# Performance work log

Hardware: AMD Instinct MI355X
Metric: run time of the kernel (lower is better)

The kernel has to match this reference:

```python
import jax, jax.numpy as jnp
import numpy as np

B, N, D_MODEL = 16, 65536, 512
NBUCKETS = 11
BN_EPS = 1e-5
LN_EPS = 1e-5


def setup_inputs() -> dict:
    key = jax.random.key(0)
    ks = jax.random.split(key, 12)
    def w(k, shape, fan_in):
        return jax.random.normal(k, shape, jnp.float32) * (1.0 / np.sqrt(fan_in))
    return {
        "x": jax.random.normal(ks[0], (B, N, 3), jnp.float32),
        "w1": w(ks[1], (3, 64), 3),   "b1": jnp.zeros((64,), jnp.float32),
        "g1": jnp.ones((64,), jnp.float32),  "be1": jnp.zeros((64,), jnp.float32),
        "w2": w(ks[2], (64, 128), 64), "b2": jnp.zeros((128,), jnp.float32),
        "g2": jnp.ones((128,), jnp.float32), "be2": jnp.zeros((128,), jnp.float32),
        "w3": w(ks[3], (128, 256), 128), "b3": jnp.zeros((256,), jnp.float32),
        "g3": jnp.ones((256,), jnp.float32), "be3": jnp.zeros((256,), jnp.float32),
        "wp": w(ks[4], (518, D_MODEL), 518), "bp": jnp.zeros((D_MODEL,), jnp.float32),
        "g_ln": jnp.ones((D_MODEL,), jnp.float32), "b_ln": jnp.zeros((D_MODEL,), jnp.float32),
    }


def _bn(h, g, b):
    # BatchNorm1d in training mode: biased variance over the flattened batch axis
    m = jnp.mean(h, axis=0)
    v = jnp.mean((h - m) ** 2, axis=0)
    return (h - m) * jax.lax.rsqrt(v + BN_EPS) * g + b


def reference(x, w1, b1, g1, be1, w2, b2, g2, be2, w3, b3, g3, be3, wp, bp, g_ln, b_ln):
    Bb, Nn, _ = x.shape
    x_flat = x.reshape(Bb * Nn, 3)
    h = jax.nn.relu(_bn(x_flat @ w1 + b1, g1, be1))
    h = jax.nn.relu(_bn(h @ w2 + b2, g2, be2))
    h = jax.nn.relu(_bn(h @ w3 + b3, g3, be3))
    feat = h.reshape(Bb, Nn, 256)

    # y-bucket histogram means of (x, z) coordinates, vectorized via segment_sum
    y = x[:, :, 1]
    y_min = jnp.min(y, axis=1, keepdims=True)
    y_max = jnp.max(y, axis=1, keepdims=True)
    y_norm = (y - y_min) / (y_max - y_min + 1e-6)
    buckets = jnp.clip((y_norm * 10).astype(jnp.int32), 0, NBUCKETS - 1)  # (B,N) in [0,10]
    seg = (jnp.arange(Bb, dtype=jnp.int32)[:, None] * NBUCKETS + buckets).reshape(-1)
    nseg = Bb * NBUCKETS
    sx = jax.ops.segment_sum(x[:, :, 0].reshape(-1), seg, num_segments=nseg)
    sz = jax.ops.segment_sum(x[:, :, 2].reshape(-1), seg, num_segments=nseg)
    cnt = jax.ops.segment_sum(jnp.ones((Bb * Nn,), jnp.float32), seg, num_segments=nseg)
    denom = jnp.maximum(cnt, 1.0)
    cx = (sx / denom).reshape(Bb, NBUCKETS)
    cz = (sz / denom).reshape(Bb, NBUCKETS)
    x_centers = jnp.take_along_axis(cx, buckets, axis=1)  # (B,N)
    z_centers = jnp.take_along_axis(cz, buckets, axis=1)

    dx = x[:, :, 0] - x_centers
    dz = x[:, :, 2] - z_centers
    theta = jnp.arctan2(dz, dx)
    r = jnp.sqrt(dx ** 2 + dz ** 2)
    spatial = jnp.stack([jnp.sin(theta), jnp.cos(theta), r], axis=-1)  # (B,N,3)

    feat = jnp.concatenate([feat, spatial], axis=-1)  # (B,N,259)
    feat_max = jnp.max(feat, axis=1)
    feat_avg = jnp.mean(feat, axis=1)
    feat_cat = jnp.concatenate([feat_max, feat_avg], axis=1)  # (B,518)

    out = feat_cat @ wp + bp
    mu = jnp.mean(out, axis=-1, keepdims=True)
    var = jnp.mean((out - mu) ** 2, axis=-1, keepdims=True)
    return (out - mu) * jax.lax.rsqrt(var + LN_EPS) * g_ln + b_ln
```

## Files before the change

kernel.cpp:

```cpp
#include <hip/hip_runtime.h>
#include <stdint.h>

#define B_    16
#define N_    65536
#define NPTS  (B_*N_)
#define NBK   11
#define NFEAT 259
#define NF    ((float)NPTS)

typedef float f32x4 __attribute__((ext_vector_type(4)));
typedef short s16x8 __attribute__((ext_vector_type(8)));
union frag_u { s16x8 v; unsigned u[4]; };
union x24_u  { float4 v4[6]; float f[24]; };

enum {
  OFF_YMINF = 16,
  OFF_YMAXF = 32,
  OFF_A1    = 64,
  OFF_C1    = 128,
  OFF_A2    = 192,
  OFF_C2    = 320,
  OFF_CX    = 448,
  OFF_CZ    = 624,
  OFF_A3    = 800,
  OFF_C3    = 1056,
  OFF_GC    = 2048,
  OFF_G1S   = 6144,
  OFF_H3C   = 6400,
  OFF_PSTR  = 16384,
  OFF_PBKT  = 24576,
  OFF_PSPA  = 43008,
  OFF_PG    = 49152,
  OFF_PGS   = 2146304,
  OFF_PH3   = 2179072,
  OFF_PPOOL = 3227648
};

__device__ __forceinline__ float wave_sum(float v){
  #pragma unroll
  for (int m=32;m>=1;m>>=1) v += __shfl_xor(v,m,64);
  return v;
}
__device__ __forceinline__ float wave_max(float v){
  #pragma unroll
  for (int m=32;m>=1;m>>=1) v = fmaxf(v,__shfl_xor(v,m,64));
  return v;
}
__device__ __forceinline__ float wave_min(float v){
  #pragma unroll
  for (int m=32;m>=1;m>>=1) v = fminf(v,__shfl_xor(v,m,64));
  return v;
}
__device__ __forceinline__ unsigned short bf16_bits(float f){
  unsigned u=__float_as_uint(f);
  u += 0x7FFFu + ((u>>16)&1u);
  return (unsigned short)(u>>16);
}
__device__ __forceinline__ unsigned cvt_pk_bf16(float lo, float hi){
  unsigned r;
  asm("v_cvt_pk_bf16_f32 %0, %1, %2" : "=v"(r) : "v"(lo), "v"(hi));
  return r;
}

__global__ __launch_bounds__(256) void k_stream0(const float* __restrict__ x,
                                                 float* __restrict__ ws){
  __shared__ float red[4][12];
  const int t=threadIdx.x, l=t&63, w=t>>6;
  const int bid=blockIdx.x;
  const float4* xv=(const float4*)(x + (size_t)bid*2048*3);
  float s0=0,s1=0,s2=0,q00=0,q01=0,q02=0,q11=0,q12=0,q22=0;
  float ymn=3.4e38f, ymx=-3.4e38f;
  #pragma unroll
  for (int i=0;i<2;i++){
    const int vi=(i*256+t)*3;
    const float4 a=xv[vi], b4=xv[vi+1], c=xv[vi+2];
    float X[4]={a.x,a.w,b4.z,c.y};
    float Y[4]={a.y,b4.x,b4.w,c.z};
    float Z[4]={a.z,b4.y,c.x,c.w};
    #pragma unroll
    for (int p=0;p<4;p++){
      s0+=X[p]; s1+=Y[p]; s2+=Z[p];
      q00=fmaf(X[p],X[p],q00); q01=fmaf(X[p],Y[p],q01); q02=fmaf(X[p],Z[p],q02);
      q11=fmaf(Y[p],Y[p],q11); q12=fmaf(Y[p],Z[p],q12); q22=fmaf(Z[p],Z[p],q22);
      ymn=fminf(ymn,Y[p]); ymx=fmaxf(ymx,Y[p]);
    }
  }
  s0=wave_sum(s0); s1=wave_sum(s1); s2=wave_sum(s2);
  q00=wave_sum(q00); q01=wave_sum(q01); q02=wave_sum(q02);
  q11=wave_sum(q11); q12=wave_sum(q12); q22=wave_sum(q22);
  ymn=wave_min(ymn); ymx=wave_max(ymx);
  if (l==0){
    red[w][0]=s0; red[w][1]=s1; red[w][2]=s2;
    red[w][3]=q00; red[w][4]=q01; red[w][5]=q02;
    red[w][6]=q11; red[w][7]=q12; red[w][8]=q22;
    red[w][9]=ymn; red[w][10]=ymx;
  }
  __syncthreads();
  if (t<11){
    const float v0=red[0][t],v1=red[1][t],v2=red[2][t],v3=red[3][t];
    float r;
    if (t==9)       r=fminf(fminf(v0,v1),fminf(v2,v3));
    else if (t==10) r=fmaxf(fmaxf(v0,v1),fmaxf(v2,v3));
    else            r=v0+v1+v2+v3;
    ws[OFF_PSTR+bid*16+t]=r;
  }
}

__global__ void k_finA(const float* __restrict__ w1, const float* __restrict__ b1,
                       const float* __restrict__ gm, const float* __restrict__ bt,
                       float* __restrict__ ws){
  __shared__ float sums[9];
  const int t=threadIdx.x;
  if (t<9){
    float s=0.f;
    #pragma unroll 8
    for (int blk=0;blk<512;blk++) s+=ws[OFF_PSTR+blk*16+t];
    sums[t]=s;
  }
  if (t>=32&&t<48){
    const int b=t-32; float m=3.4e38f;
    #pragma unroll 8
    for (int blk=0;blk<32;blk++) m=fminf(m,ws[OFF_PSTR+(b*32+blk)*16+9]);
    ws[OFF_YMINF+b]=m;
  }
  if (t>=48&&t<64){
    const int b=t-48; float m=-3.4e38f;
    #pragma unroll 8
    for (int blk=0;blk<32;blk++) m=fmaxf(m,ws[OFF_PSTR+(b*32+blk)*16+10]);
    ws[OFF_YMAXF+b]=m;
  }
  __syncthreads();
  if (t<64){
    const float i_n=1.f/NF;
    const float w0=w1[t], wa=w1[64+t], wb=w1[128+t];
    const float ms=(w0*sums[0]+wa*sums[1]+wb*sums[2])*i_n;
    const float es=(w0*w0*sums[3]+wa*wa*sums[6]+wb*wb*sums[8]
                   +2.f*(w0*wa*sums[4]+w0*wb*sums[5]+wa*wb*sums[7]))*i_n;
    const float var=es-ms*ms;
    const float a=gm[t]/sqrtf(var+1e-5f);
    ws[OFF_A1+t]=a; ws[OFF_C1+t]=bt[t]-(ms+b1[t])*a;
  }
}

__global__ __launch_bounds__(256) void k_bucket(const float* __restrict__ x,
                                                float* __restrict__ ws){
  __shared__ float red[4][12];
  const int t=threadIdx.x, l=t&63, w=t>>6;
  const int bid=blockIdx.x, b=bid>>5;
  const float ymn=ws[OFF_YMINF+b], ymx=ws[OFF_YMAXF+b];
  const float4* xv=(const float4*)(x + (size_t)bid*2048*3);
  float sxl[NBK], szl[NBK], cntl[NBK];
  #pragma unroll
  for (int k=0;k<NBK;k++){ sxl[k]=0.f; szl[k]=0.f; cntl[k]=0.f; }
  #pragma unroll
  for (int i=0;i<2;i++){
    const int vi=(i*256+t)*3;
    const float4 a=xv[vi], b4=xv[vi+1], c=xv[vi+2];
    float X[4]={a.x,a.w,b4.z,c.y};
    float Y[4]={a.y,b4.x,b4.w,c.z};
    float Z[4]={a.z,b4.y,c.x,c.w};
    #pragma unroll
    for (int p=0;p<4;p++){
      const float yn=(Y[p]-ymn)/(ymx-ymn+1e-6f);
      int bk=(int)(yn*10.f); bk = bk<0?0:(bk>10?10:bk);
      #pragma unroll
      for (int k=0;k<NBK;k++){
        const bool m=(bk==k);
        sxl[k]+= m?X[p]:0.f; szl[k]+= m?Z[p]:0.f; cntl[k]+= m?1.f:0.f;
      }
    }
  }
  #pragma unroll
  for (int k=0;k<NBK;k++){
    const float s=wave_sum(sxl[k]);
    if (l==0) red[w][k]=s;
  }
  __syncthreads();
  if (t<NBK) ws[OFF_PBKT+bid*36+t]=red[0][t]+red[1][t]+red[2][t]+red[3][t];
  __syncthreads();
  #pragma unroll
  for (int k=0;k<NBK;k++){
    const float z=wave_sum(szl[k]);
    if (l==0) red[w][k]=z;
  }
  __syncthreads();
  if (t<NBK) ws[OFF_PBKT+bid*36+11+t]=red[0][t]+red[1][t]+red[2][t]+red[3][t];
  __syncthreads();
  #pragma unroll
  for (int k=0;k<NBK;k++){
    const float c=wave_sum(cntl[k]);
    if (l==0) red[w][k]=c;
  }
  __syncthreads();
  if (t<NBK) ws[OFF_PBKT+bid*36+22+t]=red[0][t]+red[1][t]+red[2][t]+red[3][t];
}

__global__ __launch_bounds__(256) void k_spatial(const float* __restrict__ x,
                                                 float* __restrict__ ws){
  __shared__ float red[4][8];
  const int t=threadIdx.x, l=t&63, w=t>>6;
  const int bid=blockIdx.x, b=bid>>5;
  const float ymn=ws[OFF_YMINF+b], ymx=ws[OFF_YMAXF+b];
  const float4* xv=(const float4*)(x + (size_t)bid*2048*3);
  float mx[3]={-3.4e38f,-3.4e38f,-3.4e38f}, sm[3]={0.f,0.f,0.f};
  #pragma unroll
  for (int i=0;i<2;i++){
    const int vi=(i*256+t)*3;
    const float4 a=xv[vi], b4=xv[vi+1], c=xv[vi+2];
    float X[4]={a.x,a.w,b4.z,c.y};
    float Y[4]={a.y,b4.x,b4.w,c.z};
    float Z[4]={a.z,b4.y,c.x,c.w};
    #pragma unroll
    for (int p=0;p<4;p++){
      const float yn=(Y[p]-ymn)/(ymx-ymn+1e-6f);
      int bk=(int)(yn*10.f); bk = bk<0?0:(bk>10?10:bk);
      const float dx=X[p]-ws[OFF_CX+b*NBK+bk];
      const float dz=Z[p]-ws[OFF_CZ+b*NBK+bk];
      const float r=sqrtf(fmaf(dx,dx,dz*dz));
      const float sn=(r>0.f)?(dz/r):0.f;
      const float cs=(r>0.f)?(dx/r):1.f;
      mx[0]=fmaxf(mx[0],sn); sm[0]+=sn;
      mx[1]=fmaxf(mx[1],cs); sm[1]+=cs;
      mx[2]=fmaxf(mx[2],r);  sm[2]+=r;
// ... 60 lines not shown
    if (!(w&1)){
      #pragma unroll
      for (int j=0;j<8;j++) s1+=gA[j];
    }
  }
  #pragma unroll
  for (int q=0;q<4;q++){
    ws[OFF_PG + (size_t)((16*ti+4*lg+q)*64 + 16*tj0+lr)*512 + bid]=acc0[q];
    ws[OFF_PG + (size_t)((16*ti+4*lg+q)*64 + 16*tj1+lr)*512 + bid]=acc1[q];
  }
  if (!(w&1)){
    s1+=__shfl_xor(s1,16); s1+=__shfl_xor(s1,32);
    if (l<16) ws[OFF_PGS + (16*ti+lr)*512 + bid]=s1;
  }
}

__global__ __launch_bounds__(256) void k_redG(float* __restrict__ ws){
  __shared__ float red[256];
  const int t=threadIdx.x, blk=blockIdx.x;
  if (blk<64){
    const int e=blk*64+(t>>2), q=t&3;
    float s=0.f;
    const float* p=ws+OFF_PG+(size_t)e*512+q*128;
    #pragma unroll 8
    for (int i=0;i<128;i++) s+=p[i];
    red[t]=s; __syncthreads();
    if (q==0) ws[OFF_GC+e]=red[t]+red[t+1]+red[t+2]+red[t+3];
  } else {
    const int f=t>>2, q=t&3;
    float s=0.f;
    const float* p=ws+OFF_PGS+(size_t)f*512+q*128;
    #pragma unroll 8
    for (int i=0;i<128;i++) s+=p[i];
    red[t]=s; __syncthreads();
    if (q==0) ws[OFF_G1S+f]=red[t]+red[t+1]+red[t+2]+red[t+3];
  }
}

__global__ __launch_bounds__(256) void k_finB2(
    const float* __restrict__ w2, const float* __restrict__ b2,
    const float* __restrict__ gm, const float* __restrict__ bt,
    float* __restrict__ ws){
  __shared__ float red[256];
  __shared__ float red2[64];
  const int t=threadIdx.x, j=blockIdx.x;
  if (j<128){
    float acc=0.f;
    #pragma unroll
    for (int p=0;p<16;p++){
      const int idx=p*256+t;
      const int r=idx>>6, c=idx&63;
      acc += w2[r*128+j]*ws[OFF_GC+r*64+c]*w2[c*128+j];
    }
    red[t]=acc;
    if (t<64) red2[t]=w2[t*128+j]*ws[OFF_G1S+t];
    __syncthreads();
    for (int s=128;s>0;s>>=1){ if (t<s) red[t]+=red[t+s]; __syncthreads(); }
    if (t<32) red2[t]+=red2[t+32];
    __syncthreads();
    if (t==0){
      float sw=0.f;
      #pragma unroll
      for (int i=0;i<32;i++) sw+=red2[i];
      const float i_n=1.f/NF;
      const float bj=b2[j];
      const float m=sw*i_n+bj;
      const float e2=(red[0]+2.f*bj*sw)*i_n+bj*bj;
      const float var=e2-m*m;
      const float a=gm[j]/sqrtf(var+1e-5f);
      ws[OFF_A2+j]=a; ws[OFF_C2+j]=bt[j]-m*a;
    }
  } else {
    if (t<176){
      const int b=t/NBK, k=t-b*NBK;
      float sx=0.f, sz=0.f, cn=0.f;
      #pragma unroll 8
      for (int blk=0;blk<32;blk++){
        const int p=OFF_PBKT+(b*32+blk)*36;
        sx+=ws[p+k]; sz+=ws[p+11+k]; cn+=ws[p+22+k];
      }
      const float d=fmaxf(cn,1.f);
      ws[OFF_CX+t]=sx/d; ws[OFF_CZ+t]=sz/d;
    }
  }
}

template<int MODE>
__global__ __launch_bounds__(512,2) void k_mlp(
    const float* __restrict__ x,
    const float* __restrict__ w1, const float* __restrict__ b1,
    const float* __restrict__ w2, const float* __restrict__ b2,
    const float* __restrict__ w3, const float* __restrict__ b3,
    float* __restrict__ ws)
{
  __shared__ short g1t[128*72];
  __shared__ short g2t[128*136];
  const int t=threadIdx.x, w=t>>6, l=t&63, lg=l>>4, lr=l&15;
  const int bid=blockIdx.x, b=bid>>6, chunk=bid&63;
  const int ptg=w&1, fgrp=w>>1;
  char* g1c=(char*)g1t; char* g2c=(char*)g2t;

  const int fg=l&7, pj=(l>>3)&7;
  const float* a1=ws+OFF_A1; const float* c1=ws+OFF_C1;
  float w1f[3][8], b1f[8];
  #pragma unroll
  for (int i=0;i<8;i++){
    const int f=8*fg+i; const float a=a1[f];
    #pragma unroll
    for (int q=0;q<3;q++) w1f[q][i]=w1[q*64+f]*a;
    b1f[i]=b1[f]*a+c1[f];
  }

  s16x8 w2f[2][2]; float b2v[2][4];
  #pragma unroll
  for (int j=0;j<2;j++){
    const int col2=(2*fgrp+j)*16+lr;
    const float sc2=ws[OFF_A2+col2];
    #pragma unroll
    for (int kt=0;kt<2;kt++)
      #pragma unroll
      for (int i=0;i<8;i++)
        w2f[j][kt][i]=(short)bf16_bits(w2[(kt*32+8*lg+i)*128+col2]*sc2);
    #pragma unroll
    for (int r=0;r<4;r++){
      const int f2=(2*fgrp+j)*16+4*lg+r;
      b2v[j][r]=ws[OFF_A2+f2]*b2[f2]+ws[OFF_C2+f2];
    }
  }

  s16x8 w3f[4][4]; float b3v[4][4];
  #pragma unroll
  for (int j=0;j<4;j++){
    const int col3=(4*fgrp+j)*16+lr;
    const float sc3=(MODE==1)?1.f:ws[OFF_A3+col3];
    #pragma unroll
    for (int kt=0;kt<4;kt++)
      #pragma unroll
      for (int i=0;i<8;i++)
        w3f[j][kt][i]=(short)bf16_bits(w3[(kt*32+8*lg+i)*256+col3]*sc3);
    #pragma unroll
    for (int r=0;r<4;r++){
      const int f3=(4*fgrp+j)*16+4*lg+r;
      b3v[j][r]=(MODE==1)? b3[f3] : (ws[OFF_A3+f3]*b3[f3]+ws[OFF_C3+f3]);
    }
  }

  float aS[4][4], aQ[4][4];
  #pragma unroll
  for (int j=0;j<4;j++)
    #pragma unroll
    for (int r=0;r<4;r++){ aS[j][r]=(MODE==2)?-3.4e38f:0.f; aQ[j][r]=0.f; }

  const int base=b*N_+chunk*1024;
  const int ptl=16*w+2*pj;

  float c0[3], c1v[3], n0[3], n1[3];
  {
    const float* xp=&x[(size_t)(base+ptl)*3];
    #pragma unroll
    for (int q=0;q<3;q++){ c0[q]=xp[q]; c1v[q]=xp[3+q]; }
  }

  #pragma unroll 1
  for (int it=0; it<8; ++it){
    #pragma unroll
    for (int s=0;s<2;s++){
      const float x0=s?c1v[0]:c0[0], x1v=s?c1v[1]:c0[1], x2=s?c1v[2]:c0[2];
      unsigned pk[4];
      #pragma unroll
      for (int i=0;i<4;i++){
        float v0=b1f[2*i], v1=b1f[2*i+1];
        v0=fmaf(x0,w1f[0][2*i],v0);  v1=fmaf(x0,w1f[0][2*i+1],v1);
        v0=fmaf(x1v,w1f[1][2*i],v0); v1=fmaf(x1v,w1f[1][2*i+1],v1);
        v0=fmaf(x2,w1f[2][2*i],v0);  v1=fmaf(x2,w1f[2][2*i+1],v1);
        pk[i]=cvt_pk_bf16(fmaxf(v0,0.f),fmaxf(v1,0.f));
      }
      *(int4*)(g1c + (ptl+s)*144 + fg*16) = make_int4(pk[0],pk[1],pk[2],pk[3]);
    }
    if (it<7){
      const float* xp=&x[(size_t)(base+(it+1)*128+ptl)*3];
      #pragma unroll
      for (int q=0;q<3;q++){ n0[q]=xp[q]; n1[q]=xp[3+q]; }
    }
    __syncthreads();
    #pragma unroll
    for (int pt=0;pt<4;pt++){
      const int row=ptg*64+pt*16+lr;
      const s16x8 bf0=*(const s16x8*)(g1c + row*144 + lg*16);
      const s16x8 bf1=*(const s16x8*)(g1c + row*144 + 64 + lg*16);
      #pragma unroll
      for (int j=0;j<2;j++){
        f32x4 acc={b2v[j][0],b2v[j][1],b2v[j][2],b2v[j][3]};
        acc=__builtin_amdgcn_mfma_f32_16x16x32_bf16(w2f[j][0],bf0,acc,0,0,0);
        acc=__builtin_amdgcn_mfma_f32_16x16x32_bf16(w2f[j][1],bf1,acc,0,0,0);
        const unsigned lo=cvt_pk_bf16(fmaxf(acc[0],0.f),fmaxf(acc[1],0.f));
        const unsigned hi=cvt_pk_bf16(fmaxf(acc[2],0.f),fmaxf(acc[3],0.f));
        *(uint2*)(g2c + row*272 + fgrp*64 + j*32 + lg*8) = make_uint2(lo,hi);
      }
    }
    __syncthreads();
    #pragma unroll 1
    for (int pt=0;pt<4;pt++){
      const int row=ptg*64+pt*16+lr;
      const s16x8 bf0=*(const s16x8*)(g2c + row*272 + lg*16);
      const s16x8 bf1=*(const s16x8*)(g2c + row*272 + 64 + lg*16);
      const s16x8 bf2=*(const s16x8*)(g2c + row*272 + 128 + lg*16);
      const s16x8 bf3=*(const s16x8*)(g2c + row*272 + 192 + lg*16);
      #pragma unroll
      for (int j=0;j<4;j++){
        f32x4 a3={b3v[j][0],b3v[j][1],b3v[j][2],b3v[j][3]};
        a3=__builtin_amdgcn_mfma_f32_16x16x32_bf16(w3f[j][0],bf0,a3,0,0,0);
        a3=__builtin_amdgcn_mfma_f32_16x16x32_bf16(w3f[j][1],bf1,a3,0,0,0);
        a3=__builtin_amdgcn_mfma_f32_16x16x32_bf16(w3f[j][2],bf2,a3,0,0,0);
        a3=__builtin_amdgcn_mfma_f32_16x16x32_bf16(w3f[j][3],bf3,a3,0,0,0);
        #pragma unroll
        for (int r=0;r<4;r++){
          if (MODE==1){
            const float h=a3[r]; aS[j][r]+=h; aQ[j][r]=fmaf(h,h,aQ[j][r]);
          } else {
            const float g=fmaxf(a3[r],0.f);
            aS[j][r]=fmaxf(aS[j][r],g); aQ[j][r]+=g;
          }
        }
      }
    }
    #pragma unroll
    for (int q=0;q<3;q++){ c0[q]=n0[q]; c1v[q]=n1[q]; }
  }

  #pragma unroll
  for (int j=0;j<4;j++)
    #pragma unroll
    for (int r=0;r<4;r++){
      const int f3=(4*fgrp+j)*16+4*lg+r;
      if (MODE==1){
        float s=aS[j][r], q=aQ[j][r];
        #pragma unroll
        for (int m=1;m<16;m<<=1){ s+=__shfl_xor(s,m); q+=__shfl_xor(q,m); }
        if (lr==0){
          const int slot=bid*2+ptg;
          ws[OFF_PH3 + (size_t)f3*2048 + slot]=s;
          ws[OFF_PH3 + (size_t)(256+f3)*2048 + slot]=q;
        }
      } else {
        float mxv=aS[j][r], s=aQ[j][r];
        #pragma unroll
        for (int m=1;m<16;m<<=1){ mxv=fmaxf(mxv,__shfl_xor(mxv,m)); s+=__shfl_xor(s,m); }
        if (lr==0){
          const int slot=chunk*2+ptg;
          ws[OFF_PPOOL + (size_t)b*512*128 + (size_t)f3*128 + slot]=mxv;
          ws[OFF_PPOOL + (size_t)b*512*128 + (size_t)(256+f3)*128 + slot]=s;
        }
      }
    }
}

__global__ __launch_bounds__(256) void k_redH3(float* __restrict__ ws){
  __shared__ float red[256];
  const int t=threadIdx.x, blk=blockIdx.x;
  const int col=blk*16+(t>>4), part=t&15;
  float s=0.f;
  const float* p=ws+OFF_PH3+(size_t)col*2048+part*128;
  #pragma unroll 8
  for (int i=0;i<128;i++) s+=p[i];
  red[t]=s; __syncthreads();
  if (part==0){
    float r=0.f;
    #pragma unroll
    for (int i=0;i<16;i++) r+=red[(t&~15)+i];
    ws[OFF_H3C+col]=r;
  }
}

__global__ void k_finC(const float* __restrict__ gm, const float* __restrict__ bt,
                       float* __restrict__ ws){
  const int t=threadIdx.x;
  if (t<256){
    const float i_n=1.f/NF;
    const float m=ws[OFF_H3C+t]*i_n;
    const float v=ws[OFF_H3C+256+t]*i_n-m*m;
    const float a=gm[t]/sqrtf(v+1e-5f);
    ws[OFF_A3+t]=a; ws[OFF_C3+t]=bt[t]-m*a;
  }
}

__global__ __launch_bounds__(256) void k_final(
    const float* __restrict__ wp, const float* __restrict__ bp,
    const float* __restrict__ gln, const float* __restrict__ bln,
    float* __restrict__ out, const float* __restrict__ ws)
{
  __shared__ float feat[518];
  __shared__ float red[256];
  const int b=blockIdx.x, t=threadIdx.x;
  {
    float fm=-3.4e38f, fs=0.f;
    const float* pm =ws+OFF_PPOOL+(size_t)b*512*128+(size_t)t*128;
    const float* psu=ws+OFF_PPOOL+(size_t)b*512*128+(size_t)(256+t)*128;
    #pragma unroll 8
    for (int s=0;s<128;s++){ fm=fmaxf(fm,pm[s]); fs+=psu[s]; }
    feat[t]=fm; feat[NFEAT+t]=fs*(1.f/65536.f);
  }
  if (t<3){
    float fm=-3.4e38f, fs=0.f;
    #pragma unroll 4
    for (int blk=0;blk<32;blk++){
      const int p=OFF_PSPA+(b*32+blk)*8;
      fm=fmaxf(fm,ws[p+t]);
      fs+=ws[p+4+t];
    }
    feat[256+t]=fm; feat[NFEAT+256+t]=fs*(1.f/65536.f);
  }
  __syncthreads();
  float o0=bp[t], o1=bp[t+256];
  #pragma unroll 4
  for (int i=0;i<518;i++){
    const float f=feat[i];
    o0=fmaf(f, wp[i*512+t],     o0);
    o1=fmaf(f, wp[i*512+t+256], o1);
  }
  red[t]=o0+o1; __syncthreads();
  for (int s=128;s>0;s>>=1){ if (t<s) red[t]+=red[t+s]; __syncthreads(); }
  const float mu=red[0]*(1.f/512.f);
  __syncthreads();
  const float d0=o0-mu, d1=o1-mu;
  red[t]=d0*d0+d1*d1; __syncthreads();
  for (int s=128;s>0;s>>=1){ if (t<s) red[t]+=red[t+s]; __syncthreads(); }
  const float var=red[0]*(1.f/512.f);
  const float rs=1.f/sqrtf(var+1e-5f);
  out[b*512+t]     = d0*rs*gln[t]    +bln[t];
  out[b*512+t+256] = d1*rs*gln[t+256]+bln[t+256];
}

extern "C" void kernel_launch(void* const* d_in, const int* in_sizes, int n_in,
                              void* d_out, int out_size, void* d_ws, size_t ws_size,
                              hipStream_t stream)
{
  const float* x  =(const float*)d_in[0];
  const float* w1 =(const float*)d_in[1];
  const float* b1 =(const float*)d_in[2];
  const float* gm1=(const float*)d_in[3];
  const float* be1=(const float*)d_in[4];
  const float* w2 =(const float*)d_in[5];
  const float* b2 =(const float*)d_in[6];
  const float* gm2=(const float*)d_in[7];
  const float* be2=(const float*)d_in[8];
  const float* w3 =(const float*)d_in[9];
  const float* b3 =(const float*)d_in[10];
  const float* gm3=(const float*)d_in[11];
  const float* be3=(const float*)d_in[12];
  const float* wp =(const float*)d_in[13];
  const float* bp =(const float*)d_in[14];
  const float* gln=(const float*)d_in[15];
  const float* bln=(const float*)d_in[16];
  float* ws=(float*)d_ws;
  float* out=(float*)d_out;

  k_stream0<<<dim3(512), dim3(256),0,stream>>>(x,ws);
  k_finA   <<<dim3(1),   dim3(256),0,stream>>>(w1,b1,gm1,be1,ws);
  k_bucket <<<dim3(512), dim3(256),0,stream>>>(x,ws);
  k_gram   <<<dim3(512), dim3(512),0,stream>>>(x,w1,b1,ws);
  k_redG   <<<dim3(65),  dim3(256),0,stream>>>(ws);
  k_finB2  <<<dim3(129), dim3(256),0,stream>>>(w2,b2,gm2,be2,ws);
  k_spatial<<<dim3(512), dim3(256),0,stream>>>(x,ws);
  k_mlp<1> <<<dim3(1024),dim3(512),0,stream>>>(x,w1,b1,w2,b2,w3,b3,ws);
  k_redH3  <<<dim3(32),  dim3(256),0,stream>>>(ws);
  k_finC   <<<dim3(1),   dim3(256),0,stream>>>(gm3,be3,ws);
  k_mlp<2> <<<dim3(1024),dim3(512),0,stream>>>(x,w1,b1,w2,b2,w3,b3,ws);
  k_final  <<<dim3(16),  dim3(256),0,stream>>>(wp,bp,gln,bln,out,ws);
}
```

Before: 446.9 us.

## Derive layer-3 BN statistics from layer-2 Gram matrix instead of full MLP pass

```diff
diff --git a/kernel.cpp b/kernel.cpp
--- a/kernel.cpp
+++ b/kernel.cpp
@@ -26,14 +26,16 @@
   OFF_C3    = 1056,
   OFF_GC    = 2048,
   OFF_G1S   = 6144,
-  OFF_H3C   = 6400,
   OFF_PSTR  = 16384,
   OFF_PBKT  = 24576,
   OFF_PSPA  = 43008,
   OFF_PG    = 49152,
   OFF_PGS   = 2146304,
-  OFF_PH3   = 2179072,
-  OFF_PPOOL = 3227648
+  OFF_PPOOL = 3227648,
+  OFF_PG2   = 4300800,
+  OFF_PG2S  = 12689408,
+  OFF_G2C   = 12754944,
+  OFF_G2S   = 12771328
 };
 
 __device__ __forceinline__ float wave_sum(float v){
@@ -368,8 +370,170 @@
   }
 }
 
-template<int MODE>
-__global__ __launch_bounds__(512,2) void k_mlp(
+__global__ __launch_bounds__(512,1) void k_gram2(
+    const float* __restrict__ x,
+    const float* __restrict__ w1, const float* __restrict__ b1,
+    const float* __restrict__ w2, const float* __restrict__ b2,
+    float* __restrict__ ws)
+{
+  const int t=threadIdx.x, w=t>>6, l=t&63, lg=l>>4, lr=l&15;
+  const int bid=blockIdx.x;
+  const float* A1=ws+OFF_A1; const float* C1=ws+OFF_C1;
+  const float* A2=ws+OFF_A2; const float* C2=ws+OFF_C2;
+
+  float w1f[2][3][8], b1f[2][8];
+  #pragma unroll
+  for (int kt=0;kt<2;kt++)
+    #pragma unroll
+    for (int i=0;i<8;i++){
+      const int f=kt*32+8*lg+i; const float a=A1[f];
+      w1f[kt][0][i]=w1[f]*a; w1f[kt][1][i]=w1[64+f]*a; w1f[kt][2][i]=w1[128+f]*a;
+      b1f[kt][i]=b1[f]*a+C1[f];
+    }
+
+  s16x8 w2f[8][2]; float b2v[8];
+  #pragma unroll
+  for (int tt=0;tt<8;tt++){
+    const int col2=16*tt+lr;
+    const float sc2=A2[col2];
+    #pragma unroll
+    for (int kt=0;kt<2;kt++)
+      #pragma unroll
+      for (int i=0;i<8;i++)
+        w2f[tt][kt][i]=(short)bf16_bits(w2[(kt*32+8*lg+i)*128+col2]*sc2);
+    b2v[tt]=A2[col2]*b2[col2]+C2[col2];
+  }
+
+  f32x4 gacc[8];
+  float sacc[8];
+  #pragma unroll
+  for (int j=0;j<8;j++){ gacc[j]=(f32x4){0.f,0.f,0.f,0.f}; sacc[j]=0.f; }
+
+  const float* xb = x + (size_t)bid*2048*3;
+
+  #pragma unroll 1
+  for (int win=0; win<64; ++win){
+    frag_u a1f[2][2];
+    #pragma unroll
+    for (int s=0;s<2;s++){
+      const int pt=win*32+s*16+lr;
+      const float x0=xb[pt*3+0], x1v=xb[pt*3+1], x2=xb[pt*3+2];
+      #pragma unroll
+      for (int kt=0;kt<2;kt++){
+        float h[8];
+        #pragma unroll
+        for (int i=0;i<8;i++){
+          float v=b1f[kt][i];
+          v=fmaf(x0,w1f[kt][0][i],v); v=fmaf(x1v,w1f[kt][1][i],v); v=fmaf(x2,w1f[kt][2][i],v);
+          h[i]=fmaxf(v,0.f);
+        }
+        #pragma unroll
+        for (int m=0;m<4;m++) a1f[s][kt].u[m]=cvt_pk_bf16(h[2*m],h[2*m+1]);
+      }
+    }
+    s16x8 fB[8]; frag_u fA;
+    #pragma unroll
+    for (int tt=0;tt<8;tt++){
+      f32x4 d0={b2v[tt],b2v[tt],b2v[tt],b2v[tt]};
+      f32x4 d1=d0;
+      d0=__builtin_amdgcn_mfma_f32_16x16x32_bf16(a1f[0][0].v,w2f[tt][0],d0,0,0,0);
+      d0=__builtin_amdgcn_mfma_f32_16x16x32_bf16(a1f[0][1].v,w2f[tt][1],d0,0,0,0);
+      d1=__builtin_amdgcn_mfma_f32_16x16x32_bf16(a1f[1][0].v,w2f[tt][0],d1,0,0,0);
+      d1=__builtin_amdgcn_mfma_f32_16x16x32_bf16(a1f[1][1].v,w2f[tt][1],d1,0,0,0);
+      float e0[4], e1[4];
+      #pragma unroll
+      for (int r=0;r<4;r++){
+        e0[r]=fmaxf(d0[r],0.f); e1[r]=fmaxf(d1[r],0.f);
+        sacc[tt]+=e0[r]+e1[r];
+      }
+      const unsigned p0a=cvt_pk_bf16(e0[0],e0[1]), p0b=cvt_pk_bf16(e0[2],e0[3]);
+      const unsigned p1a=cvt_pk_bf16(e1[0],e1[1]), p1b=cvt_pk_bf16(e1[2],e1[3]);
+      frag_u fr;
+      #pragma unroll
+      for (int m=0;m<4;m++){
+        const int src=lr + 16*(2*(lg&1)+(m>>1));
+        const unsigned q0=(m&1)?p0b:p0a;
+        const unsigned q1=(m&1)?p1b:p1a;
+        const unsigned u0=(unsigned)__shfl((int)q0,src,64);
+        const unsigned u1=(unsigned)__shfl((int)q1,src,64);
+        fr.u[m]=(lg<2)?u0:u1;
+      }
+      fB[tt]=fr.v;
+      if (tt==w) fA=fr;
+    }
+    #pragma unroll
+    for (int j=0;j<8;j++)
+      gacc[j]=__builtin_amdgcn_mfma_f32_16x16x32_bf16(fA.v,fB[j],gacc[j],0,0,0);
+  }
+
+  #pragma unroll
+  for (int j=0;j<8;j++)
+    #pragma unroll
+    for (int r=0;r<4;r++)
+      ws[OFF_PG2 + (size_t)bid*16384 + (16*w+4*lg+r)*128 + 16*j+lr]=gacc[j][r];
+  #pragma unroll
+  for (int tt=0;tt<8;tt++){
+    float v=sacc[tt];
+    v+=__shfl_xor(v,16); v+=__shfl_xor(v,32);
+    if (l<16) ws[OFF_PG2S + (size_t)bid*128 + 16*tt+lr]=v;
+  }
+}
+
+__global__ __launch_bounds__(256) void k_redG2(float* __restrict__ ws){
+  const int t=threadIdx.x, blk=blockIdx.x;
+  if (blk<64){
+    const int e=blk*256+t;
+    float s=0.f;
+    #pragma unroll 8
+    for (int b=0;b<512;b++) s+=ws[OFF_PG2+(size_t)b*16384+e];
+    ws[OFF_G2C+e]=s;
+  } else {
+    if (t<128){
+      float s=0.f;
+      #pragma unroll 8
+      for (int b=0;b<512;b++) s+=ws[OFF_PG2S+(size_t)b*128+t];
+      ws[OFF_G2S+t]=s;
+    }
+  }
+}
+
+__global__ __launch_bounds__(256) void k_finC2(
+    const float* __restrict__ w3, const float* __restrict__ b3,
+    const float* __restrict__ gm, const float* __restrict__ bt,
+    float* __restrict__ ws){
+  __shared__ float red[256];
+  __shared__ float red2[128];
+  const int t=threadIdx.x, j=blockIdx.x;
+  float acc=0.f;
+  #pragma unroll 4
+  for (int it=0; it<64; ++it){
+    const int idx=it*256+t;
+    const int r=idx>>7, c=idx&127;
+    acc += w3[r*256+j]*ws[OFF_G2C+idx]*w3[c*256+j];
+  }
+  red[t]=acc;
+  if (t<128) red2[t]=w3[t*256+j]*ws[OFF_G2S+t];
+  __syncthreads();
+  for (int s=128;s>0;s>>=1){ if (t<s) red[t]+=red[t+s]; __syncthreads(); }
+  if (t<64) red2[t]+=red2[t+64];
+  __syncthreads();
+  if (t<32) red2[t]+=red2[t+32];
+  __syncthreads();
+  if (t==0){
+    float sw=0.f;
+    #pragma unroll
+    for (int i=0;i<32;i++) sw+=red2[i];
+    const float i_n=1.f/NF;
+    const float bj=b3[j];
+    const float m=sw*i_n+bj;
+    const float e2=(red[0]+2.f*bj*sw)*i_n+bj*bj;
+    const float var=e2-m*m;
+    const float a=gm[j]/sqrtf(var+1e-5f);
+    ws[OFF_A3+j]=a; ws[OFF_C3+j]=bt[j]-m*a;
+  }
+}
+
+__global__ __launch_bounds__(512,2) void k_mlp2(
     const float* __restrict__ x,
     const float* __restrict__ w1, const float* __restrict__ b1,
     const float* __restrict__ w2, const float* __restrict__ b2,
@@ -415,7 +579,7 @@
   #pragma unroll
   for (int j=0;j<4;j++){
     const int col3=(4*fgrp+j)*16+lr;
-    const float sc3=(MODE==1)?1.f:ws[OFF_A3+col3];
+    const float sc3=ws[OFF_A3+col3];
     #pragma unroll
     for (int kt=0;kt<4;kt++)
       #pragma unroll
@@ -424,7 +588,7 @@
     #pragma unroll
     for (int r=0;r<4;r++){
       const int f3=(4*fgrp+j)*16+4*lg+r;
-      b3v[j][r]=(MODE==1)? b3[f3] : (ws[OFF_A3+f3]*b3[f3]+ws[OFF_C3+f3]);
+      b3v[j][r]=ws[OFF_A3+f3]*b3[f3]+ws[OFF_C3+f3];
     }
   }
 
@@ -432,7 +596,7 @@
   #pragma unroll
   for (int j=0;j<4;j++)
     #pragma unroll
-    for (int r=0;r<4;r++){ aS[j][r]=(MODE==2)?-3.4e38f:0.f; aQ[j][r]=0.f; }
+    for (int r=0;r<4;r++){ aS[j][r]=-3.4e38f; aQ[j][r]=0.f; }
 
   const int base=b*N_+chunk*1024;
   const int ptl=16*w+2*pj;
@@ -498,12 +662,8 @@
         a3=__builtin_amdgcn_mfma_f32_16x16x32_bf16(w3f[j][3],bf3,a3,0,0,0);
         #pragma unroll
         for (int r=0;r<4;r++){
-          if (MODE==1){
-            const float h=a3[r]; aS[j][r]+=h; aQ[j][r]=fmaf(h,h,aQ[j][r]);
-          } else {
-            const float g=fmaxf(a3[r],0.f);
-            aS[j][r]=fmaxf(aS[j][r],g); aQ[j][r]+=g;
-          }
+          const float g=fmaxf(a3[r],0.f);
+          aS[j][r]=fmaxf(aS[j][r],g); aQ[j][r]+=g;
         }
       }
     }
@@ -516,55 +676,15 @@
     #pragma unroll
     for (int r=0;r<4;r++){
       const int f3=(4*fgrp+j)*16+4*lg+r;
-      if (MODE==1){
-        float s=aS[j][r], q=aQ[j][r];
-        #pragma unroll
-        for (int m=1;m<16;m<<=1){ s+=__shfl_xor(s,m); q+=__shfl_xor(q,m); }
-        if (lr==0){
-          const int slot=bid*2+ptg;
-          ws[OFF_PH3 + (size_t)f3*2048 + slot]=s;
-          ws[OFF_PH3 + (size_t)(256+f3)*2048 + slot]=q;
-        }
-      } else {
-        float mxv=aS[j][r], s=aQ[j][r];
-        #pragma unroll
-        for (int m=1;m<16;m<<=1){ mxv=fmaxf(mxv,__shfl_xor(mxv,m)); s+=__shfl_xor(s,m); }
-        if (lr==0){
-          const int slot=chunk*2+ptg;
-          ws[OFF_PPOOL + (size_t)b*512*128 + (size_t)f3*128 + slot]=mxv;
-          ws[OFF_PPOOL + (size_t)b*512*128 + (size_t)(256+f3)*128 + slot]=s;
-        }
-      }
-    }
-}
-
-__global__ __launch_bounds__(256) void k_redH3(float* __restrict__ ws){
-  __shared__ float red[256];
-  const int t=threadIdx.x, blk=blockIdx.x;
-  const int col=blk*16+(t>>4), part=t&15;
-  float s=0.f;
-  const float* p=ws+OFF_PH3+(size_t)col*2048+part*128;
-  #pragma unroll 8
-  for (int i=0;i<128;i++) s+=p[i];
-  red[t]=s; __syncthreads();
-  if (part==0){
-    float r=0.f;
-    #pragma unroll
-    for (int i=0;i<16;i++) r+=red[(t&~15)+i];
-    ws[OFF_H3C+col]=r;
-  }
-}
-
-__global__ void k_finC(const float* __restrict__ gm, const float* __restrict__ bt,
-                       float* __restrict__ ws){
-  const int t=threadIdx.x;
-  if (t<256){
-    const float i_n=1.f/NF;
-    const float m=ws[OFF_H3C+t]*i_n;
-    const float v=ws[OFF_H3C+256+t]*i_n-m*m;
-    const float a=gm[t]/sqrtf(v+1e-5f);
-    ws[OFF_A3+t]=a; ws[OFF_C3+t]=bt[t]-m*a;
-  }
+      float mxv=aS[j][r], s=aQ[j][r];
+      #pragma unroll
+      for (int m=1;m<16;m<<=1){ mxv=fmaxf(mxv,__shfl_xor(mxv,m)); s+=__shfl_xor(s,m); }
+      if (lr==0){
+        const int slot=chunk*2+ptg;
+        ws[OFF_PPOOL + (size_t)b*512*128 + (size_t)f3*128 + slot]=mxv;
+        ws[OFF_PPOOL + (size_t)b*512*128 + (size_t)(256+f3)*128 + slot]=s;
+      }
+    }
 }
 
 __global__ __launch_bounds__(256) void k_final(
@@ -644,10 +764,10 @@
   k_gram   <<<dim3(512), dim3(512),0,stream>>>(x,w1,b1,ws);
   k_redG   <<<dim3(65),  dim3(256),0,stream>>>(ws);
   k_finB2  <<<dim3(129), dim3(256),0,stream>>>(w2,b2,gm2,be2,ws);
+  k_gram2  <<<dim3(512), dim3(512),0,stream>>>(x,w1,b1,w2,b2,ws);
+  k_redG2  <<<dim3(65),  dim3(256),0,stream>>>(ws);
+  k_finC2  <<<dim3(256), dim3(256),0,stream>>>(w3,b3,gm3,be3,ws);
   k_spatial<<<dim3(512), dim3(256),0,stream>>>(x,ws);
-  k_mlp<1> <<<dim3(1024),dim3(512),0,stream>>>(x,w1,b1,w2,b2,w3,b3,ws);
-  k_redH3  <<<dim3(32),  dim3(256),0,stream>>>(ws);
-  k_finC   <<<dim3(1),   dim3(256),0,stream>>>(gm3,be3,ws);
-  k_mlp<2> <<<dim3(1024),dim3(512),0,stream>>>(x,w1,b1,w2,b2,w3,b3,ws);
+  k_mlp2   <<<dim3(1024),dim3(512),0,stream>>>(x,w1,b1,w2,b2,w3,b3,ws);
   k_final  <<<dim3(16),  dim3(256),0,stream>>>(wp,bp,gln,bln,out,ws);
 }
```

After: 782.6 us. +75.1%, slower.

## Spill layer-3 pre-BN activations to bf16 buffer instead of recomputing MLP

Applied to the files above, without the earlier changes.

```diff
diff --git a/kernel.cpp b/kernel.cpp
--- a/kernel.cpp
+++ b/kernel.cpp
@@ -27,14 +27,18 @@
   OFF_GC    = 2048,
   OFF_G1S   = 6144,
   OFF_H3C   = 6400,
+  OFF_PMAX  = 8192,
+  OFF_PSUM  = 12288,
   OFF_PSTR  = 16384,
   OFF_PBKT  = 24576,
   OFF_PSPA  = 43008,
   OFF_PG    = 49152,
+  OFF_PH3   = 65536,
+  OFF_H3B   = 1114112,
   OFF_PGS   = 2146304,
-  OFF_PH3   = 2179072,
   OFF_PPOOL = 3227648
 };
+#define SPILL_BYTES ((size_t)(OFF_H3B + (size_t)128*NPTS) * 4)
 
 __device__ __forceinline__ float wave_sum(float v){
   #pragma unroll
@@ -365,6 +369,195 @@
       const float d=fmaxf(cn,1.f);
       ws[OFF_CX+t]=sx/d; ws[OFF_CZ+t]=sz/d;
     }
+  }
+}
+
+
+__global__ __launch_bounds__(512,2) void k_mlpS(
+    const float* __restrict__ x,
+    const float* __restrict__ w1, const float* __restrict__ b1,
+    const float* __restrict__ w2, const float* __restrict__ b2,
+    const float* __restrict__ w3, const float* __restrict__ b3,
+    float* __restrict__ ws)
+{
+  __shared__ short g1t[128*72];
+  __shared__ short g2t[128*136];
+  const int t=threadIdx.x, w=t>>6, l=t&63, lg=l>>4, lr=l&15;
+  const int bid=blockIdx.x, b=bid>>6, chunk=bid&63;
+  const int ptg=w&1, fgrp=w>>1;
+  char* g1c=(char*)g1t; char* g2c=(char*)g2t;
+  unsigned* h3p=(unsigned*)(ws+OFF_H3B);
+
+  const int fg=l&7, pj=(l>>3)&7;
+  const float* a1=ws+OFF_A1; const float* c1=ws+OFF_C1;
+  float w1f[3][8], b1f[8];
+  #pragma unroll
+  for (int i=0;i<8;i++){
+    const int f=8*fg+i; const float a=a1[f];
+    #pragma unroll
+    for (int q=0;q<3;q++) w1f[q][i]=w1[q*64+f]*a;
+    b1f[i]=b1[f]*a+c1[f];
+  }
+
+  s16x8 w2f[2][2]; float b2v[2][4];
+  #pragma unroll
+  for (int j=0;j<2;j++){
+    const int col2=(2*fgrp+j)*16+lr;
+    const float sc2=ws[OFF_A2+col2];
+    #pragma unroll
+    for (int kt=0;kt<2;kt++)
+      #pragma unroll
+      for (int i=0;i<8;i++)
+        w2f[j][kt][i]=(short)bf16_bits(w2[(kt*32+8*lg+i)*128+col2]*sc2);
+    #pragma unroll
+    for (int r=0;r<4;r++){
+      const int f2=(2*fgrp+j)*16+4*lg+r;
+      b2v[j][r]=ws[OFF_A2+f2]*b2[f2]+ws[OFF_C2+f2];
+    }
+  }
+
+  s16x8 w3f[4][4]; float b3v[4][4];
+  #pragma unroll
+  for (int j=0;j<4;j++){
+    const int col3=(4*fgrp+j)*16+lr;
+    #pragma unroll
+    for (int kt=0;kt<4;kt++)
+      #pragma unroll
+      for (int i=0;i<8;i++)
+        w3f[j][kt][i]=(short)bf16_bits(w3[(kt*32+8*lg+i)*256+col3]);
+    #pragma unroll
+    for (int r=0;r<4;r++)
+      b3v[j][r]=b3[(4*fgrp+j)*16+4*lg+r];
+  }
+
+  float aS[4][4], aQ[4][4];
+  #pragma unroll
+  for (int j=0;j<4;j++)
+    #pragma unroll
+    for (int r=0;r<4;r++){ aS[j][r]=0.f; aQ[j][r]=0.f; }
+
+  const int base=b*N_+chunk*1024;
+  const int ptl=16*w+2*pj;
+
+  float c0[3], c1v[3], n0[3], n1[3];
+  {
+    const float* xp=&x[(size_t)(base+ptl)*3];
+    #pragma unroll
+    for (int q=0;q<3;q++){ c0[q]=xp[q]; c1v[q]=xp[3+q]; }
+  }
+
+  #pragma unroll 1
+  for (int it=0; it<8; ++it){
+    #pragma unroll
+    for (int s=0;s<2;s++){
+      const float x0=s?c1v[0]:c0[0], x1v=s?c1v[1]:c0[1], x2=s?c1v[2]:c0[2];
+      unsigned pk[4];
+      #pragma unroll
+      for (int i=0;i<4;i++){
+        float v0=b1f[2*i], v1=b1f[2*i+1];
+        v0=fmaf(x0,w1f[0][2*i],v0);  v1=fmaf(x0,w1f[0][2*i+1],v1);
+        v0=fmaf(x1v,w1f[1][2*i],v0); v1=fmaf(x1v,w1f[1][2*i+1],v1);
+        v0=fmaf(x2,w1f[2][2*i],v0);  v1=fmaf(x2,w1f[2][2*i+1],v1);
+        pk[i]=cvt_pk_bf16(fmaxf(v0,0.f),fmaxf(v1,0.f));
+      }
+      *(int4*)(g1c + (ptl+s)*144 + fg*16) = make_int4(pk[0],pk[1],pk[2],pk[3]);
+    }
+    if (it<7){
+      const float* xp=&x[(size_t)(base+(it+1)*128+ptl)*3];
+      #pragma unroll
+      for (int q=0;q<3;q++){ n0[q]=xp[q]; n1[q]=xp[3+q]; }
+    }
+    __syncthreads();
+    #pragma unroll
+    for (int pt=0;pt<4;pt++){
+      const int row=ptg*64+pt*16+lr;
+      const s16x8 bf0=*(const s16x8*)(g1c + row*144 + lg*16);
+      const s16x8 bf1=*(const s16x8*)(g1c + row*144 + 64 + lg*16);
+      #pragma unroll
+      for (int j=0;j<2;j++){
+        f32x4 acc={b2v[j][0],b2v[j][1],b2v[j][2],b2v[j][3]};
+        acc=__builtin_amdgcn_mfma_f32_16x16x32_bf16(w2f[j][0],bf0,acc,0,0,0);
+        acc=__builtin_amdgcn_mfma_f32_16x16x32_bf16(w2f[j][1],bf1,acc,0,0,0);
+        const unsigned lo=cvt_pk_bf16(fmaxf(acc[0],0.f),fmaxf(acc[1],0.f));
+        const unsigned hi=cvt_pk_bf16(fmaxf(acc[2],0.f),fmaxf(acc[3],0.f));
+        *(uint2*)(g2c + row*272 + fgrp*64 + j*32 + lg*8) = make_uint2(lo,hi);
+      }
+    }
+    __syncthreads();
+    #pragma unroll 1
+    for (int pt=0;pt<4;pt++){
+      const int row=ptg*64+pt*16+lr;
+      const int gp=base+it*128+row;
+      const s16x8 bf0=*(const s16x8*)(g2c + row*272 + lg*16);
+      const s16x8 bf1=*(const s16x8*)(g2c + row*272 + 64 + lg*16);
+      const s16x8 bf2=*(const s16x8*)(g2c + row*272 + 128 + lg*16);
+      const s16x8 bf3=*(const s16x8*)(g2c + row*272 + 192 + lg*16);
+      #pragma unroll
+      for (int j=0;j<4;j++){
+        f32x4 a3={b3v[j][0],b3v[j][1],b3v[j][2],b3v[j][3]};
+        a3=__builtin_amdgcn_mfma_f32_16x16x32_bf16(w3f[j][0],bf0,a3,0,0,0);
+        a3=__builtin_amdgcn_mfma_f32_16x16x32_bf16(w3f[j][1],bf1,a3,0,0,0);
+        a3=__builtin_amdgcn_mfma_f32_16x16x32_bf16(w3f[j][2],bf2,a3,0,0,0);
+        a3=__builtin_amdgcn_mfma_f32_16x16x32_bf16(w3f[j][3],bf3,a3,0,0,0);
+        const int fpair=(4*fgrp+j)*8+2*lg;
+        h3p[(size_t)fpair*NPTS+gp]    =cvt_pk_bf16(a3[0],a3[1]);
+        h3p[(size_t)(fpair+1)*NPTS+gp]=cvt_pk_bf16(a3[2],a3[3]);
+        #pragma unroll
+        for (int r=0;r<4;r++){
+          const float h=a3[r]; aS[j][r]+=h; aQ[j][r]=fmaf(h,h,aQ[j][r]);
+        }
+      }
+    }
+    #pragma unroll
+    for (int q=0;q<3;q++){ c0[q]=n0[q]; c1v[q]=n1[q]; }
+  }
+
+  #pragma unroll
+  for (int j=0;j<4;j++)
+    #pragma unroll
+    for (int r=0;r<4;r++){
+      const int f3=(4*fgrp+j)*16+4*lg+r;
+      float s=aS[j][r], q=aQ[j][r];
+      #pragma unroll
+      for (int m=1;m<16;m<<=1){ s+=__shfl_xor(s,m); q+=__shfl_xor(q,m); }
+      if (lr==0){
+        const int slot=bid*2+ptg;
+        ws[OFF_PH3 + (size_t)f3*2048 + slot]=s;
+        ws[OFF_PH3 + (size_t)(256+f3)*2048 + slot]=q;
+      }
+    }
+}
+
+__global__ __launch_bounds__(256) void k_pool(float* __restrict__ ws){
+  const int t=threadIdx.x, w=t>>6, l=t&63;
+  const int bid=blockIdx.x, b=bid>>5;
+  const int fp=(bid&31)*4+w;
+  const unsigned* h3p=(const unsigned*)(ws+OFF_H3B);
+  const int f0=2*fp, f1=f0+1;
+  const float a0=ws[OFF_A3+f0], c0=ws[OFF_C3+f0];
+  const float a1=ws[OFF_A3+f1], c1=ws[OFF_C3+f1];
+  const uint4* rowp=(const uint4*)(h3p + (size_t)fp*NPTS + (size_t)b*N_);
+  float m0=-3.4e38f,s0=0.f,m1=-3.4e38f,s1=0.f;
+  #pragma unroll 4
+  for (int i=0;i<256;i++){
+    const uint4 v=rowp[(size_t)i*64+l];
+    const unsigned uu[4]={v.x,v.y,v.z,v.w};
+    #pragma unroll
+    for (int q=0;q<4;q++){
+      const unsigned u=uu[q];
+      const float h0=__uint_as_float(u<<16);
+      const float h1=__uint_as_float(u&0xffff0000u);
+      const float g0=fmaxf(fmaf(h0,a0,c0),0.f);
+      const float g1=fmaxf(fmaf(h1,a1,c1),0.f);
+      m0=fmaxf(m0,g0); s0+=g0;
+      m1=fmaxf(m1,g1); s1+=g1;
+    }
+  }
+  m0=wave_max(m0); s0=wave_sum(s0);
+  m1=wave_max(m1); s1=wave_sum(s1);
+  if (l==0){
+    ws[OFF_PMAX+b*256+f0]=m0; ws[OFF_PSUM+b*256+f0]=s0;
+    ws[OFF_PMAX+b*256+f1]=m1; ws[OFF_PSUM+b*256+f1]=s1;
   }
 }
 
@@ -567,6 +760,7 @@
   }
 }
 
+template<int SP>
 __global__ __launch_bounds__(256) void k_final(
     const float* __restrict__ wp, const float* __restrict__ bp,
     const float* __restrict__ gln, const float* __restrict__ bln,
@@ -575,7 +769,10 @@
   __shared__ float feat[518];
   __shared__ float red[256];
   const int b=blockIdx.x, t=threadIdx.x;
-  {
+  if (SP){
+    feat[t]      =ws[OFF_PMAX+b*256+t];
+    feat[NFEAT+t]=ws[OFF_PSUM+b*256+t]*(1.f/65536.f);
+  } else {
     float fm=-3.4e38f, fs=0.f;
     const float* pm =ws+OFF_PPOOL+(size_t)b*512*128+(size_t)t*128;
     const float* psu=ws+OFF_PPOOL+(size_t)b*512*128+(size_t)(256+t)*128;
@@ -637,6 +834,7 @@
   const float* bln=(const float*)d_in[16];
   float* ws=(float*)d_ws;
   float* out=(float*)d_out;
+  const bool spill = (ws_size >= SPILL_BYTES);
 
   k_stream0<<<dim3(512), dim3(256),0,stream>>>(x,ws);
   k_finA   <<<dim3(1),   dim3(256),0,stream>>>(w1,b1,gm1,be1,ws);
@@ -645,9 +843,17 @@
   k_redG   <<<dim3(65),  dim3(256),0,stream>>>(ws);
   k_finB2  <<<dim3(129), dim3(256),0,stream>>>(w2,b2,gm2,be2,ws);
   k_spatial<<<dim3(512), dim3(256),0,stream>>>(x,ws);
-  k_mlp<1> <<<dim3(1024),dim3(512),0,stream>>>(x,w1,b1,w2,b2,w3,b3,ws);
-  k_redH3  <<<dim3(32),  dim3(256),0,stream>>>(ws);
-  k_finC   <<<dim3(1),   dim3(256),0,stream>>>(gm3,be3,ws);
-  k_mlp<2> <<<dim3(1024),dim3(512),0,stream>>>(x,w1,b1,w2,b2,w3,b3,ws);
-  k_final  <<<dim3(16),  dim3(256),0,stream>>>(wp,bp,gln,bln,out,ws);
-}
+  if (spill){
+    k_mlpS   <<<dim3(1024),dim3(512),0,stream>>>(x,w1,b1,w2,b2,w3,b3,ws);
+    k_redH3  <<<dim3(32),  dim3(256),0,stream>>>(ws);
+    k_finC   <<<dim3(1),   dim3(256),0,stream>>>(gm3,be3,ws);
+    k_pool   <<<dim3(512), dim3(256),0,stream>>>(ws);
+    k_final<1><<<dim3(16), dim3(256),0,stream>>>(wp,bp,gln,bln,out,ws);
+  } else {
+    k_mlp<1> <<<dim3(1024),dim3(512),0,stream>>>(x,w1,b1,w2,b2,w3,b3,ws);
+    k_redH3  <<<dim3(32),  dim3(256),0,stream>>>(ws);
+    k_finC   <<<dim3(1),   dim3(256),0,stream>>>(gm3,be3,ws);
+    k_mlp<2> <<<dim3(1024),dim3(512),0,stream>>>(x,w1,b1,w2,b2,w3,b3,ws);
+    k_final<0><<<dim3(16), dim3(256),0,stream>>>(wp,bp,gln,bln,out,ws);
+  }
+}
```

Result: no change. 448.8 us (+0.4%).

## Precompute layer-1 bf16 activations in a separate kernel and double-buffer layer-2 LDS

Applied to the files above, without the earlier changes.

```diff
diff --git a/kernel.cpp b/kernel.cpp
--- a/kernel.cpp
+++ b/kernel.cpp
@@ -31,9 +31,10 @@
   OFF_PBKT  = 24576,
   OFF_PSPA  = 43008,
   OFF_PG    = 49152,
+  OFF_PH3   = 65536,
   OFF_PGS   = 2146304,
-  OFF_PH3   = 2179072,
-  OFF_PPOOL = 3227648
+  OFF_PPOOL = 3227648,
+  OFF_G1H   = 4300800
 };
 
 __device__ __forceinline__ float wave_sum(float v){
@@ -139,6 +140,39 @@
     const float var=es-ms*ms;
     const float a=gm[t]/sqrtf(var+1e-5f);
     ws[OFF_A1+t]=a; ws[OFF_C1+t]=bt[t]-(ms+b1[t])*a;
+  }
+}
+
+__global__ __launch_bounds__(256) void k_g1(const float* __restrict__ x,
+                                            const float* __restrict__ w1,
+                                            const float* __restrict__ b1,
+                                            float* __restrict__ ws){
+  const int t=threadIdx.x, fg=t&7, pr=t>>3;
+  const int bid=blockIdx.x;
+  short* g1h=(short*)(ws+OFF_G1H);
+  const float* A1=ws+OFF_A1; const float* C1=ws+OFF_C1;
+  float w1f[3][8], b1f[8];
+  #pragma unroll
+  for (int i=0;i<8;i++){
+    const int f=8*fg+i; const float a=A1[f];
+    #pragma unroll
+    for (int q=0;q<3;q++) w1f[q][i]=w1[q*64+f]*a;
+    b1f[i]=b1[f]*a+C1[f];
+  }
+  #pragma unroll 2
+  for (int i=0;i<16;i++){
+    const int pt=bid*512 + i*32 + pr;
+    const float x0=x[pt*3+0], x1v=x[pt*3+1], x2=x[pt*3+2];
+    unsigned pk[4];
+    #pragma unroll
+    for (int m=0;m<4;m++){
+      float v0=b1f[2*m], v1=b1f[2*m+1];
+      v0=fmaf(x0,w1f[0][2*m],v0);  v1=fmaf(x0,w1f[0][2*m+1],v1);
+      v0=fmaf(x1v,w1f[1][2*m],v0); v1=fmaf(x1v,w1f[1][2*m+1],v1);
+      v0=fmaf(x2,w1f[2][2*m],v0);  v1=fmaf(x2,w1f[2][2*m+1],v1);
+      pk[m]=cvt_pk_bf16(fmaxf(v0,0.f),fmaxf(v1,0.f));
+    }
+    *(int4*)(g1h + (size_t)pt*64 + fg*8) = make_int4(pk[0],pk[1],pk[2],pk[3]);
   }
 }
 
@@ -370,29 +404,16 @@
 
 template<int MODE>
 __global__ __launch_bounds__(512,2) void k_mlp(
-    const float* __restrict__ x,
-    const float* __restrict__ w1, const float* __restrict__ b1,
     const float* __restrict__ w2, const float* __restrict__ b2,
     const float* __restrict__ w3, const float* __restrict__ b3,
     float* __restrict__ ws)
 {
-  __shared__ short g1t[128*72];
-  __shared__ short g2t[128*136];
+  __shared__ short g2t[2*128*136];
   const int t=threadIdx.x, w=t>>6, l=t&63, lg=l>>4, lr=l&15;
   const int bid=blockIdx.x, b=bid>>6, chunk=bid&63;
   const int ptg=w&1, fgrp=w>>1;
-  char* g1c=(char*)g1t; char* g2c=(char*)g2t;
-
-  const int fg=l&7, pj=(l>>3)&7;
-  const float* a1=ws+OFF_A1; const float* c1=ws+OFF_C1;
-  float w1f[3][8], b1f[8];
-  #pragma unroll
-  for (int i=0;i<8;i++){
-    const int f=8*fg+i; const float a=a1[f];
-    #pragma unroll
-    for (int q=0;q<3;q++) w1f[q][i]=w1[q*64+f]*a;
-    b1f[i]=b1[f]*a+c1[f];
-  }
+  char* g2base=(char*)g2t;
+  const short* g1h=(const short*)(ws+OFF_G1H);
 
   s16x8 w2f[2][2]; float b2v[2][4];
   #pragma unroll
@@ -434,43 +455,18 @@
     #pragma unroll
     for (int r=0;r<4;r++){ aS[j][r]=(MODE==2)?-3.4e38f:0.f; aQ[j][r]=0.f; }
 
-  const int base=b*N_+chunk*1024;
-  const int ptl=16*w+2*pj;
-
-  float c0[3], c1v[3], n0[3], n1[3];
-  {
-    const float* xp=&x[(size_t)(base+ptl)*3];
-    #pragma unroll
-    for (int q=0;q<3;q++){ c0[q]=xp[q]; c1v[q]=xp[3+q]; }
-  }
-
+  const size_t base=(size_t)b*N_+(size_t)chunk*1024;
+
+  int cur=0;
   #pragma unroll 1
   for (int it=0; it<8; ++it){
-    #pragma unroll
-    for (int s=0;s<2;s++){
-      const float x0=s?c1v[0]:c0[0], x1v=s?c1v[1]:c0[1], x2=s?c1v[2]:c0[2];
-      unsigned pk[4];
-      #pragma unroll
-      for (int i=0;i<4;i++){
-        float v0=b1f[2*i], v1=b1f[2*i+1];
-        v0=fmaf(x0,w1f[0][2*i],v0);  v1=fmaf(x0,w1f[0][2*i+1],v1);
-        v0=fmaf(x1v,w1f[1][2*i],v0); v1=fmaf(x1v,w1f[1][2*i+1],v1);
-        v0=fmaf(x2,w1f[2][2*i],v0);  v1=fmaf(x2,w1f[2][2*i+1],v1);
-        pk[i]=cvt_pk_bf16(fmaxf(v0,0.f),fmaxf(v1,0.f));
-      }
-      *(int4*)(g1c + (ptl+s)*144 + fg*16) = make_int4(pk[0],pk[1],pk[2],pk[3]);
-    }
-    if (it<7){
-      const float* xp=&x[(size_t)(base+(it+1)*128+ptl)*3];
-      #pragma unroll
-      for (int q=0;q<3;q++){ n0[q]=xp[q]; n1[q]=xp[3+q]; }
-    }
-    __syncthreads();
+    char* g2cur=g2base + cur*34816;
     #pragma unroll
     for (int pt=0;pt<4;pt++){
       const int row=ptg*64+pt*16+lr;
-      const s16x8 bf0=*(const s16x8*)(g1c + row*144 + lg*16);
-      const s16x8 bf1=*(const s16x8*)(g1c + row*144 + 64 + lg*16);
+      const size_t gp=base + it*128 + row;
+      const s16x8 bf0=*(const s16x8*)(g1h + gp*64 + lg*8);
+      const s16x8 bf1=*(const s16x8*)(g1h + gp*64 + 32 + lg*8);
       #pragma unroll
       for (int j=0;j<2;j++){
         f32x4 acc={b2v[j][0],b2v[j][1],b2v[j][2],b2v[j][3]};
@@ -478,17 +474,17 @@
         acc=__builtin_amdgcn_mfma_f32_16x16x32_bf16(w2f[j][1],bf1,acc,0,0,0);
         const unsigned lo=cvt_pk_bf16(fmaxf(acc[0],0.f),fmaxf(acc[1],0.f));
         const unsigned hi=cvt_pk_bf16(fmaxf(acc[2],0.f),fmaxf(acc[3],0.f));
-        *(uint2*)(g2c + row*272 + fgrp*64 + j*32 + lg*8) = make_uint2(lo,hi);
+        *(uint2*)(g2cur + row*272 + fgrp*64 + j*32 + lg*8) = make_uint2(lo,hi);
       }
     }
     __syncthreads();
     #pragma unroll 1
     for (int pt=0;pt<4;pt++){
       const int row=ptg*64+pt*16+lr;
-      const s16x8 bf0=*(const s16x8*)(g2c + row*272 + lg*16);
-      const s16x8 bf1=*(const s16x8*)(g2c + row*272 + 64 + lg*16);
-      const s16x8 bf2=*(const s16x8*)(g2c + row*272 + 128 + lg*16);
-      const s16x8 bf3=*(const s16x8*)(g2c + row*272 + 192 + lg*16);
+      const s16x8 bf0=*(const s16x8*)(g2cur + row*272 + lg*16);
+      const s16x8 bf1=*(const s16x8*)(g2cur + row*272 + 64 + lg*16);
+      const s16x8 bf2=*(const s16x8*)(g2cur + row*272 + 128 + lg*16);
+      const s16x8 bf3=*(const s16x8*)(g2cur + row*272 + 192 + lg*16);
       #pragma unroll
       for (int j=0;j<4;j++){
         f32x4 a3={b3v[j][0],b3v[j][1],b3v[j][2],b3v[j][3]};
@@ -507,8 +503,7 @@
         }
       }
     }
-    #pragma unroll
-    for (int q=0;q<3;q++){ c0[q]=n0[q]; c1v[q]=n1[q]; }
+    cur^=1;
   }
 
   #pragma unroll
@@ -640,14 +635,15 @@
 
   k_stream0<<<dim3(512), dim3(256),0,stream>>>(x,ws);
   k_finA   <<<dim3(1),   dim3(256),0,stream>>>(w1,b1,gm1,be1,ws);
+  k_g1     <<<dim3(2048),dim3(256),0,stream>>>(x,w1,b1,ws);
   k_bucket <<<dim3(512), dim3(256),0,stream>>>(x,ws);
   k_gram   <<<dim3(512), dim3(512),0,stream>>>(x,w1,b1,ws);
   k_redG   <<<dim3(65),  dim3(256),0,stream>>>(ws);
   k_finB2  <<<dim3(129), dim3(256),0,stream>>>(w2,b2,gm2,be2,ws);
   k_spatial<<<dim3(512), dim3(256),0,stream>>>(x,ws);
-  k_mlp<1> <<<dim3(1024),dim3(512),0,stream>>>(x,w1,b1,w2,b2,w3,b3,ws);
+  k_mlp<1> <<<dim3(1024),dim3(512),0,stream>>>(w2,b2,w3,b3,ws);
   k_redH3  <<<dim3(32),  dim3(256),0,stream>>>(ws);
   k_finC   <<<dim3(1),   dim3(256),0,stream>>>(gm3,be3,ws);
-  k_mlp<2> <<<dim3(1024),dim3(512),0,stream>>>(x,w1,b1,w2,b2,w3,b3,ws);
+  k_mlp<2> <<<dim3(1024),dim3(512),0,stream>>>(w2,b2,w3,b3,ws);
   k_final  <<<dim3(16),  dim3(256),0,stream>>>(wp,bp,gln,bln,out,ws);
 }
```

New measurement: 518.6 us. +16.0%, slower.
